# Performance work log

Hardware: AMD Instinct MI355X
Metric: run time of the kernel (lower is better)

Reference implementation:

```python
import jax, jax.numpy as jnp
import numpy as np

IN_DIM = 3
GRID_LEVEL = 7
FEAT_DIMS = 2
HIDDEN = 128
BOUND = 1.0
W0_SINE = 56.0  # n_levels**feature_dims - n_levels = 8**2 - 8
N = 131072


def setup_inputs() -> dict:
    key = jax.random.key(0)
    ks = jax.random.split(key, 10)
    return {
        "in_pos": jax.random.uniform(ks[0], (N, IN_DIM), jnp.float32, -1.0, 1.0),
        "grid_feats": jax.random.uniform(ks[1], (N, IN_DIM + GRID_LEVEL * FEAT_DIMS), jnp.float32),
        "ffn_A": jax.random.normal(ks[2], (GRID_LEVEL, FEAT_DIMS, HIDDEN), jnp.float32) * 5.0,
        "ffn_sigma": jnp.ones((GRID_LEVEL,), jnp.float32),
        "W0": jax.random.uniform(ks[3], (HIDDEN, IN_DIM), jnp.float32, -1.0 / IN_DIM, 1.0 / IN_DIM),
        "b0": jax.random.uniform(ks[4], (HIDDEN,), jnp.float32, -1.0 / IN_DIM, 1.0 / IN_DIM),
        "W_mid": jax.random.uniform(ks[5], (GRID_LEVEL, HIDDEN, HIDDEN), jnp.float32) * (2.0 * np.sqrt(6.0 / HIDDEN) / W0_SINE) - np.sqrt(6.0 / HIDDEN) / W0_SINE,
        "b_mid": jnp.zeros((GRID_LEVEL, HIDDEN), jnp.float32),
        "W_high": jax.random.uniform(ks[6], (GRID_LEVEL, HIDDEN, HIDDEN), jnp.float32) * (2.0 * np.sqrt(6.0 / HIDDEN) / W0_SINE) - np.sqrt(6.0 / HIDDEN) / W0_SINE,
        "b_high": jnp.zeros((GRID_LEVEL, HIDDEN), jnp.float32),
    }


def reference(in_pos, grid_feats, ffn_A, ffn_sigma, W0, b0, W_mid, b_mid, W_high, b_high):
    x = in_pos / BOUND                     # [N, 3], in [-1, 1]
    pos01 = (in_pos + BOUND) / (2.0 * BOUND)  # [N, 3], in [0, 1]

    # grid branch: slice off the first in_dim columns, reshape to [L, N, F]
    gx = grid_feats[..., IN_DIM:].reshape(-1, GRID_LEVEL, FEAT_DIMS).transpose(1, 0, 2)
    A = ffn_A * ffn_sigma[:, None, None]   # [L, F, H]
    grid_x = jnp.sin(jnp.einsum('lnf,lfh->lnh', gx, (2.0 * jnp.pi) * A))  # [L, N, H]

    # first SIREN layer
    x = jnp.sin(W0_SINE * (x @ W0.T + b0))  # [N, H]

    def step(carry, layer):
        x, buf = carry
        Wm, bm, Wh, bh, g = layer
        x = jnp.sin(W0_SINE * (x @ Wm.T + bm))
        x = g + x                                  # residual add of grid features
        buf = buf + jnp.sin(W0_SINE * (x @ Wh.T + bh))  # high-freq accumulation
        return (x, buf), None

    buf0 = jnp.zeros((x.shape[0], HIDDEN), x.dtype)
    (_, buf), _ = jax.lax.scan(step, (x, buf0), (W_mid, b_mid, W_high, b_high, grid_x))

    return jnp.concatenate([pos01, buf / GRID_LEVEL], axis=-1)  # [N, 3 + 128]
```

## Files before the change

### kernel.cpp

```cpp
#include <hip/hip_runtime.h>
#include <hip/hip_bf16.h>


typedef __bf16 bf16_t;
typedef __attribute__((ext_vector_type(8))) __bf16 bf16x8;
typedef __attribute__((ext_vector_type(4))) float f32x4;
typedef __attribute__((ext_vector_type(16))) float f32x16;

#define C56R 8.9126768f
#define INV7 0.14285714285714285f

#define OFF_WMF   0
#define OFF_WMFLO 229376
#define OFF_WHF   458752
#define OFF_EPM   688128

union ChunkU { bf16x8 v; unsigned int d[4]; };

__device__ __forceinline__ unsigned short bfbits(float x) {
  bf16_t b = (bf16_t)x;
  return __builtin_bit_cast(unsigned short, b);
}
__device__ __forceinline__ float bf2f(unsigned short u) {
  return __builtin_bit_cast(float, (unsigned int)u << 16);
}
__device__ __forceinline__ void pack2(float v0, float v1,
                                      unsigned int& ph, unsigned int& pl) {
  unsigned short h0 = bfbits(v0), h1 = bfbits(v1);
  ph = (unsigned int)h0 | ((unsigned int)h1 << 16);
  float l0 = v0 - bf2f(h0), l1 = v1 - bf2f(h1);
  pl = (unsigned int)bfbits(l0) | ((unsigned int)bfbits(l1) << 16);
}

__global__ void ffb_prep(const float* __restrict__ ffnA, const float* __restrict__ sigma,
                         const float* __restrict__ Wm, const float* __restrict__ bm,
                         const float* __restrict__ Wh, const float* __restrict__ bh,
                         unsigned char* __restrict__ ws) {
  int i = blockIdx.x * 256 + threadIdx.x;
  bf16_t* wmf = (bf16_t*)(ws + OFF_WMF);
  bf16_t* wml = (bf16_t*)(ws + OFF_WMFLO);
  bf16_t* whf = (bf16_t*)(ws + OFF_WHF);
  {
    int j    = i & 7;
    int lane = (i >> 3) & 63;
    int kc   = (i >> 9) & 7;
    int mt   = (i >> 12) & 3;
    int it   = i >> 14;
    int ho   = (mt << 5) + (lane & 31);
    int hin  = (kc << 4) + ((lane >> 5) << 3) + j;
    int src  = (it << 14) + (ho << 7) + hin;
    float w  = Wm[src];
    bf16_t h = (bf16_t)w;
    wmf[i] = h;
    wml[i] = (bf16_t)(w - (float)h);
    whf[i] = (bf16_t)Wh[src];
  }
  if (i < 896) {
    int r  = i & 15;
    int mt = (i >> 4) & 3;
    int hf = (i >> 6) & 1;
    int it = i >> 7;
    int h  = (mt << 5) + (r & 3) + ((r >> 2) << 3) + (hf << 2);
    float sg = sigma[it];
    f32x4 e;
    e.x = ffnA[it * 256 + h] * sg;
    e.y = ffnA[it * 256 + 128 + h] * sg;
    e.z = C56R * bm[it * 128 + h];
    e.w = C56R * bh[it * 128 + h];
    ((f32x4*)(ws + OFF_EPM))[i] = e;
  }
}

__launch_bounds__(256, 3)
__global__ void ffb_main(const float* __restrict__ pos,
                         const float* __restrict__ gfeat,
                         const float* __restrict__ W0,
                         const float* __restrict__ b0,
                         const unsigned char* __restrict__ ws,
                         float* __restrict__ out) {
  __shared__ __align__(16) unsigned char smem[48000];
  unsigned char* sX0 = smem;
  f32x4* sEPv = (f32x4*)(smem + 32768);
  float* sEPf = (float*)(smem + 32768);

  const int tid  = threadIdx.x;
  const int L    = tid & 63;
  const int sub  = tid >> 6;
  const int p    = L & 31;
  const int hf   = L >> 5;
  const int n    = (blockIdx.x << 5) + p;

  const bf16_t* __restrict__ WMH = (const bf16_t*)(ws + OFF_WMF);
  const bf16_t* __restrict__ WML = (const bf16_t*)(ws + OFF_WMFLO);
  const bf16_t* __restrict__ WHF = (const bf16_t*)(ws + OFF_WHF);
  const f32x4*  __restrict__ EPM = (const f32x4*)(ws + OFF_EPM);

  bf16x8 mh[8], ml[8], hfr[8];
  {
    const bf16_t* wh0 = WMH + (sub << 12) + (L << 3);
    const bf16_t* wl0 = WML + (sub << 12) + (L << 3);
    #pragma unroll
    for (int kc = 0; kc < 8; ++kc) {
      mh[kc] = *(const bf16x8*)(wh0 + (kc << 9));
      ml[kc] = *(const bf16x8*)(wl0 + (kc << 9));
    }
  }

  #pragma unroll
  for (int c = 0; c < 4; ++c) {
    int idx = tid + (c << 8);
    if (idx < 896) sEPv[(idx >> 4) * 17 + (idx & 15)] = EPM[idx];
  }

  const float p0 = pos[n * 3 + 0], p1 = pos[n * 3 + 1], p2 = pos[n * 3 + 2];
  if (sub == 0 && hf == 0) {
    out[(size_t)n * 131 + 0] = (p0 + 1.f) * 0.5f;
    out[(size_t)n * 131 + 1] = (p1 + 1.f) * 0.5f;
    out[(size_t)n * 131 + 2] = (p2 + 1.f) * 0.5f;
  }

  #pragma unroll
  for (int cc = 0; cc < 2; ++cc) {
    const int c = (sub << 1) + cc;
    ChunkU chi, clo;
    #pragma unroll
    for (int jp = 0; jp < 4; ++jp) {
      int h0 = (c << 4) + (hf << 3) + 2 * jp;
      float d0 = __builtin_fmaf(p2, W0[h0*3+2], __builtin_fmaf(p1, W0[h0*3+1], p0 * W0[h0*3+0]));
      float d1 = __builtin_fmaf(p2, W0[h0*3+5], __builtin_fmaf(p1, W0[h0*3+4], p0 * W0[h0*3+3]));
      float v0 = __builtin_amdgcn_sinf(C56R * (d0 + b0[h0]));
      float v1 = __builtin_amdgcn_sinf(C56R * (d1 + b0[h0 + 1]));
      pack2(v0, v1, chi.d[jp], clo.d[jp]);
    }
    *(bf16x8*)(sX0 + (c << 10) + (L << 4))        = chi.v;
    *(bf16x8*)(sX0 + 8192 + (c << 10) + (L << 4)) = clo.v;
  }
  __syncthreads();

  f32x16 buf;
  #pragma unroll
  for (int r = 0; r < 16; ++r) buf[r] = 0.f;

  #pragma unroll 1
  for (int it = 0; it < 8; ++it) {
    unsigned char* rb = sX0 + ((it & 1) << 14);
    unsigned char* wb = sX0 + (((it + 1) & 1) << 14);

    if (it > 0) {
      f32x16 acc;
      #pragma unroll
      for (int r = 0; r < 16; ++r) acc[r] = 0.f;
      #pragma unroll
      for (int kc = 0; kc < 8; ++kc) {
        bf16x8 xhc = *(const bf16x8*)(rb + (kc << 10) + (L << 4));
        acc = __builtin_amdgcn_mfma_f32_32x32x16_bf16(hfr[kc], xhc, acc, 0, 0, 0);
      }
      const int eb17 = ((((it - 1) << 1) + hf) * 4 + sub) * 17;
      #pragma unroll
      for (int r = 0; r < 16; ++r) {
        float cbh = sEPf[(eb17 + r) * 4 + 3];
        buf[r] += __builtin_amdgcn_sinf(__builtin_fmaf(acc[r], C56R, cbh));
      }
    }

    if (it < 7) {
      {
        const bf16_t* wbp = WHF + (it << 14) + (sub << 12) + (L << 3);
        #pragma unroll
        for (int kc = 0; kc < 8; ++kc)
          hfr[kc] = *(const bf16x8*)(wbp + (kc << 9));
      }

      f32x16 acc;
      #pragma unroll
      for (int r = 0; r < 16; ++r) acc[r] = 0.f;
      #pragma unroll
      for (int kc = 0; kc < 8; ++kc) {
        bf16x8 xhc = *(const bf16x8*)(rb + (kc << 10) + (L << 4));
        bf16x8 xlc = *(const bf16x8*)(rb + 8192 + (kc << 10) + (L << 4));
        acc = __builtin_amdgcn_mfma_f32_32x32x16_bf16(mh[kc], xhc, acc, 0, 0, 0);
        acc = __builtin_amdgcn_mfma_f32_32x32x16_bf16(ml[kc], xhc, acc, 0, 0, 0);
        acc = __builtin_amdgcn_mfma_f32_32x32x16_bf16(mh[kc], xlc, acc, 0, 0, 0);
      }

      if (it < 6) {
        const bf16_t* wh = WMH + ((it + 1) << 14) + (sub << 12) + (L << 3);
        const bf16_t* wl = WML + ((it + 1) << 14) + (sub << 12) + (L << 3);
        #pragma unroll
        for (int kc = 0; kc < 8; ++kc) {
          mh[kc] = *(const bf16x8*)(wh + (kc << 9));
          ml[kc] = *(const bf16x8*)(wl + (kc << 9));
        }
      }

      const float g0 = gfeat[n * 17 + 3 + 2 * it];
      const float g1 = gfeat[n * 17 + 4 + 2 * it];
      const int eb17 = (((it << 1) + hf) * 4 + sub) * 17;
      #pragma unroll
      for (int q = 0; q < 4; ++q) {
        const int r0 = q << 2;
        float v[4];
        #pragma unroll
        for (int k = 0; k < 4; ++k) {
          const int r = r0 + k;
          f32x4 e = sEPv[eb17 + r];
          float sg = __builtin_amdgcn_sinf(__builtin_amdgcn_fractf(__builtin_fmaf(g1, e.y, g0 * e.x)));
          float sm = __builtin_amdgcn_sinf(__builtin_fmaf(acc[r], C56R, e.z));
          v[k] = sg + sm;
        }
        unsigned int ph0, pl0, ph1, pl1;
        pack2(v[0], v[1], ph0, pl0);
        pack2(v[2], v[3], ph1, pl1);
        unsigned long long qh = (unsigned long long)ph0 | ((unsigned long long)ph1 << 32);
        unsigned long long ql = (unsigned long long)pl0 | ((unsigned long long)pl1 << 32);
        const int c   = (sub << 1) + (r0 >> 3);
        const int bit = (r0 >> 2) & 1;
        const int off = (c << 10) + ((p + (bit << 5)) << 4) + (hf << 3);
        *(unsigned long long*)(wb + off)        = qh;
        *(unsigned long long*)(wb + 8192 + off) = ql;
      }
      __syncthreads();
    }
  }

  float* op = out + (size_t)n * 131 + 3;
  #pragma unroll
  for (int r = 0; r < 16; ++r) {
    const int h = (sub << 5) + (r & 3) + ((r >> 2) << 3) + (hf << 2);
    op[h] = buf[r] * INV7;
  }
}

extern "C" void kernel_launch(void* const* d_in, const int* in_sizes, int n_in,
                              void* d_out, int out_size, void* d_ws, size_t ws_size,
                              hipStream_t stream) {
  (void)in_sizes; (void)n_in; (void)out_size; (void)ws_size;
  const float* pos   = (const float*)d_in[0];
  const float* gfeat = (const float*)d_in[1];
  const float* ffnA  = (const float*)d_in[2];
  const float* sigma = (const float*)d_in[3];
  const float* W0    = (const float*)d_in[4];
  const float* b0    = (const float*)d_in[5];
  const float* Wm    = (const float*)d_in[6];
  const float* bm    = (const float*)d_in[7];
  const float* Wh    = (const float*)d_in[8];
  const float* bh    = (const float*)d_in[9];
  float* out = (float*)d_out;
  unsigned char* ws = (unsigned char*)d_ws;

  hipLaunchKernelGGL(ffb_prep, dim3(448), dim3(256), 0, stream,
                     ffnA, sigma, Wm, bm, Wh, bh, ws);
  hipLaunchKernelGGL(ffb_main, dim3(4096), dim3(256), 0, stream,
                     pos, gfeat, W0, b0, ws, out);
}
```

Measured before the change: 267.7 us.

## Process two 32-point tiles per block to reuse weight fragments

Each block now handles 64 points as two 32-point tiles (A and B) that share the same register-resident weight fragments, so each weight load is amortized over twice the MFMA work. Shared memory grows to 64KB for the doubled activation ping-pong buffers, and the bias/FFN epilogue table now comes straight from global memory instead of a shared-memory copy. The high-frequency sine accumulation is deferred to after the next mid-layer MFMAs to overlap with them. Occupancy drops (launch bounds 3 to 2, grid halved) and register pressure rises with twice the accumulators.

```diff
diff --git a/kernel.cpp b/kernel.cpp
--- a/kernel.cpp
+++ b/kernel.cpp
@@ -71,29 +71,28 @@
   }
 }
 
-__launch_bounds__(256, 3)
+__launch_bounds__(256, 2)
 __global__ void ffb_main(const float* __restrict__ pos,
                          const float* __restrict__ gfeat,
                          const float* __restrict__ W0,
                          const float* __restrict__ b0,
                          const unsigned char* __restrict__ ws,
                          float* __restrict__ out) {
-  __shared__ __align__(16) unsigned char smem[48000];
-  unsigned char* sX0 = smem;
-  f32x4* sEPv = (f32x4*)(smem + 32768);
-  float* sEPf = (float*)(smem + 32768);
+  __shared__ __align__(16) unsigned char sX[65536];
 
   const int tid  = threadIdx.x;
   const int L    = tid & 63;
   const int sub  = tid >> 6;
   const int p    = L & 31;
   const int hf   = L >> 5;
-  const int n    = (blockIdx.x << 5) + p;
+  const int nA   = (blockIdx.x << 6) + p;
+  const int nB   = nA + 32;
 
   const bf16_t* __restrict__ WMH = (const bf16_t*)(ws + OFF_WMF);
   const bf16_t* __restrict__ WML = (const bf16_t*)(ws + OFF_WMFLO);
   const bf16_t* __restrict__ WHF = (const bf16_t*)(ws + OFF_WHF);
   const f32x4*  __restrict__ EPM = (const f32x4*)(ws + OFF_EPM);
+  const float*  __restrict__ EPW = (const float*)(ws + OFF_EPM);
 
   bf16x8 mh[8], ml[8], hfr[8];
   {
@@ -106,60 +105,61 @@
     }
   }
 
+  const float pA0 = pos[nA * 3 + 0], pA1 = pos[nA * 3 + 1], pA2 = pos[nA * 3 + 2];
+  const float pB0 = pos[nB * 3 + 0], pB1 = pos[nB * 3 + 1], pB2 = pos[nB * 3 + 2];
+  if (sub == 0 && hf == 0) {
+    out[(size_t)nA * 131 + 0] = (pA0 + 1.f) * 0.5f;
+    out[(size_t)nA * 131 + 1] = (pA1 + 1.f) * 0.5f;
+    out[(size_t)nA * 131 + 2] = (pA2 + 1.f) * 0.5f;
+    out[(size_t)nB * 131 + 0] = (pB0 + 1.f) * 0.5f;
+    out[(size_t)nB * 131 + 1] = (pB1 + 1.f) * 0.5f;
+    out[(size_t)nB * 131 + 2] = (pB2 + 1.f) * 0.5f;
+  }
+
   #pragma unroll
-  for (int c = 0; c < 4; ++c) {
-    int idx = tid + (c << 8);
-    if (idx < 896) sEPv[(idx >> 4) * 17 + (idx & 15)] = EPM[idx];
-  }
-
-  const float p0 = pos[n * 3 + 0], p1 = pos[n * 3 + 1], p2 = pos[n * 3 + 2];
-  if (sub == 0 && hf == 0) {
-    out[(size_t)n * 131 + 0] = (p0 + 1.f) * 0.5f;
-    out[(size_t)n * 131 + 1] = (p1 + 1.f) * 0.5f;
-    out[(size_t)n * 131 + 2] = (p2 + 1.f) * 0.5f;
-  }
-
+  for (int q = 0; q < 2; ++q) {
+    const float q0 = q ? pB0 : pA0;
+    const float q1 = q ? pB1 : pA1;
+    const float q2 = q ? pB2 : pA2;
+    unsigned char* base = sX + (q << 14);
+    #pragma unroll
+    for (int cc = 0; cc < 2; ++cc) {
+      const int c = (sub << 1) + cc;
+      ChunkU chi, clo;
+      #pragma unroll
+      for (int jp = 0; jp < 4; ++jp) {
+        int h0 = (c << 4) + (hf << 3) + 2 * jp;
+        float d0 = __builtin_fmaf(q2, W0[h0*3+2], __builtin_fmaf(q1, W0[h0*3+1], q0 * W0[h0*3+0]));
+        float d1 = __builtin_fmaf(q2, W0[h0*3+5], __builtin_fmaf(q1, W0[h0*3+4], q0 * W0[h0*3+3]));
+        float v0 = __builtin_amdgcn_sinf(C56R * (d0 + b0[h0]));
+        float v1 = __builtin_amdgcn_sinf(C56R * (d1 + b0[h0 + 1]));
+        pack2(v0, v1, chi.d[jp], clo.d[jp]);
+      }
+      *(bf16x8*)(base + (c << 10) + (L << 4))        = chi.v;
+      *(bf16x8*)(base + 8192 + (c << 10) + (L << 4)) = clo.v;
+    }
+  }
+  __syncthreads();
+
+  f32x16 bufA, bufB;
   #pragma unroll
-  for (int cc = 0; cc < 2; ++cc) {
-    const int c = (sub << 1) + cc;
-    ChunkU chi, clo;
-    #pragma unroll
-    for (int jp = 0; jp < 4; ++jp) {
-      int h0 = (c << 4) + (hf << 3) + 2 * jp;
-      float d0 = __builtin_fmaf(p2, W0[h0*3+2], __builtin_fmaf(p1, W0[h0*3+1], p0 * W0[h0*3+0]));
-      float d1 = __builtin_fmaf(p2, W0[h0*3+5], __builtin_fmaf(p1, W0[h0*3+4], p0 * W0[h0*3+3]));
-      float v0 = __builtin_amdgcn_sinf(C56R * (d0 + b0[h0]));
-      float v1 = __builtin_amdgcn_sinf(C56R * (d1 + b0[h0 + 1]));
-      pack2(v0, v1, chi.d[jp], clo.d[jp]);
-    }
-    *(bf16x8*)(sX0 + (c << 10) + (L << 4))        = chi.v;
-    *(bf16x8*)(sX0 + 8192 + (c << 10) + (L << 4)) = clo.v;
-  }
-  __syncthreads();
-
-  f32x16 buf;
-  #pragma unroll
-  for (int r = 0; r < 16; ++r) buf[r] = 0.f;
+  for (int r = 0; r < 16; ++r) { bufA[r] = 0.f; bufB[r] = 0.f; }
 
   #pragma unroll 1
   for (int it = 0; it < 8; ++it) {
-    unsigned char* rb = sX0 + ((it & 1) << 14);
-    unsigned char* wb = sX0 + (((it + 1) & 1) << 14);
-
+    unsigned char* rb  = sX + ((it & 1) << 15);
+    unsigned char* wbf = sX + (((it + 1) & 1) << 15);
+
+    f32x16 accHA, accHB;
     if (it > 0) {
-      f32x16 acc;
-      #pragma unroll
-      for (int r = 0; r < 16; ++r) acc[r] = 0.f;
+      #pragma unroll
+      for (int r = 0; r < 16; ++r) { accHA[r] = 0.f; accHB[r] = 0.f; }
       #pragma unroll
       for (int kc = 0; kc < 8; ++kc) {
-        bf16x8 xhc = *(const bf16x8*)(rb + (kc << 10) + (L << 4));
-        acc = __builtin_amdgcn_mfma_f32_32x32x16_bf16(hfr[kc], xhc, acc, 0, 0, 0);
-      }
-      const int eb17 = ((((it - 1) << 1) + hf) * 4 + sub) * 17;
-      #pragma unroll
-      for (int r = 0; r < 16; ++r) {
-        float cbh = sEPf[(eb17 + r) * 4 + 3];
-        buf[r] += __builtin_amdgcn_sinf(__builtin_fmaf(acc[r], C56R, cbh));
+        bf16x8 xA = *(const bf16x8*)(rb + (kc << 10) + (L << 4));
+        bf16x8 xB = *(const bf16x8*)(rb + 16384 + (kc << 10) + (L << 4));
+        accHA = __builtin_amdgcn_mfma_f32_32x32x16_bf16(hfr[kc], xA, accHA, 0, 0, 0);
+        accHB = __builtin_amdgcn_mfma_f32_32x32x16_bf16(hfr[kc], xB, accHB, 0, 0, 0);
       }
     }
 
@@ -171,16 +171,24 @@
           hfr[kc] = *(const bf16x8*)(wbp + (kc << 9));
       }
 
-      f32x16 acc;
-      #pragma unroll
-      for (int r = 0; r < 16; ++r) acc[r] = 0.f;
+      f32x16 accA, accB;
+      #pragma unroll
+      for (int r = 0; r < 16; ++r) { accA[r] = 0.f; accB[r] = 0.f; }
       #pragma unroll
       for (int kc = 0; kc < 8; ++kc) {
-        bf16x8 xhc = *(const bf16x8*)(rb + (kc << 10) + (L << 4));
-        bf16x8 xlc = *(const bf16x8*)(rb + 8192 + (kc << 10) + (L << 4));
-        acc = __builtin_amdgcn_mfma_f32_32x32x16_bf16(mh[kc], xhc, acc, 0, 0, 0);
-        acc = __builtin_amdgcn_mfma_f32_32x32x16_bf16(ml[kc], xhc, acc, 0, 0, 0);
-        acc = __builtin_amdgcn_mfma_f32_32x32x16_bf16(mh[kc], xlc, acc, 0, 0, 0);
+        bf16x8 xhA = *(const bf16x8*)(rb + (kc << 10) + (L << 4));
+        bf16x8 xlA = *(const bf16x8*)(rb + 8192 + (kc << 10) + (L << 4));
+        accA = __builtin_amdgcn_mfma_f32_32x32x16_bf16(mh[kc], xhA, accA, 0, 0, 0);
+        accA = __builtin_amdgcn_mfma_f32_32x32x16_bf16(ml[kc], xhA, accA, 0, 0, 0);
+        accA = __builtin_amdgcn_mfma_f32_32x32x16_bf16(mh[kc], xlA, accA, 0, 0, 0);
+      }
+      #pragma unroll
+      for (int kc = 0; kc < 8; ++kc) {
+        bf16x8 xhB = *(const bf16x8*)(rb + 16384 + (kc << 10) + (L << 4));
+        bf16x8 xlB = *(const bf16x8*)(rb + 24576 + (kc << 10) + (L << 4));
+        accB = __builtin_amdgcn_mfma_f32_32x32x16_bf16(mh[kc], xhB, accB, 0, 0, 0);
+        accB = __builtin_amdgcn_mfma_f32_32x32x16_bf16(ml[kc], xhB, accB, 0, 0, 0);
+        accB = __builtin_amdgcn_mfma_f32_32x32x16_bf16(mh[kc], xlB, accB, 0, 0, 0);
       }
 
       if (it < 6) {
@@ -193,41 +201,72 @@
         }
       }
 
-      const float g0 = gfeat[n * 17 + 3 + 2 * it];
-      const float g1 = gfeat[n * 17 + 4 + 2 * it];
-      const int eb17 = (((it << 1) + hf) * 4 + sub) * 17;
+      if (it > 0) {
+        const int ebp = ((((it - 1) << 1) + hf) * 4 + sub) * 16;
+        #pragma unroll
+        for (int r = 0; r < 16; ++r) {
+          float cbh = EPW[(ebp + r) * 4 + 3];
+          bufA[r] += __builtin_amdgcn_sinf(__builtin_fmaf(accHA[r], C56R, cbh));
+          bufB[r] += __builtin_amdgcn_sinf(__builtin_fmaf(accHB[r], C56R, cbh));
+        }
+      }
+
+      const float g0A = gfeat[nA * 17 + 3 + 2 * it];
+      const float g1A = gfeat[nA * 17 + 4 + 2 * it];
+      const float g0B = gfeat[nB * 17 + 3 + 2 * it];
+      const float g1B = gfeat[nB * 17 + 4 + 2 * it];
+      const int eb = (((it << 1) + hf) * 4 + sub) * 16;
       #pragma unroll
       for (int q = 0; q < 4; ++q) {
         const int r0 = q << 2;
-        float v[4];
+        float vA[4], vB[4];
         #pragma unroll
         for (int k = 0; k < 4; ++k) {
           const int r = r0 + k;
-          f32x4 e = sEPv[eb17 + r];
-          float sg = __builtin_amdgcn_sinf(__builtin_amdgcn_fractf(__builtin_fmaf(g1, e.y, g0 * e.x)));
-          float sm = __builtin_amdgcn_sinf(__builtin_fmaf(acc[r], C56R, e.z));
-          v[k] = sg + sm;
+          f32x4 e = EPM[eb + r];
+          float sgA = __builtin_amdgcn_sinf(__builtin_amdgcn_fractf(__builtin_fmaf(g1A, e.y, g0A * e.x)));
+          float smA = __builtin_amdgcn_sinf(__builtin_fmaf(accA[r], C56R, e.z));
+          vA[k] = sgA + smA;
+          float sgB = __builtin_amdgcn_sinf(__builtin_amdgcn_fractf(__builtin_fmaf(g1B, e.y, g0B * e.x)));
+          float smB = __builtin_amdgcn_sinf(__builtin_fmaf(accB[r], C56R, e.z));
+          vB[k] = sgB + smB;
         }
-        unsigned int ph0, pl0, ph1, pl1;
-        pack2(v[0], v[1], ph0, pl0);
-        pack2(v[2], v[3], ph1, pl1);
-        unsigned long long qh = (unsigned long long)ph0 | ((unsigned long long)ph1 << 32);
-        unsigned long long ql = (unsigned long long)pl0 | ((unsigned long long)pl1 << 32);
+        unsigned int h0, l0, h1, l1;
+        pack2(vA[0], vA[1], h0, l0);
+        pack2(vA[2], vA[3], h1, l1);
+        unsigned long long qhA = (unsigned long long)h0 | ((unsigned long long)h1 << 32);
+        unsigned long long qlA = (unsigned long long)l0 | ((unsigned long long)l1 << 32);
+        pack2(vB[0], vB[1], h0, l0);
+        pack2(vB[2], vB[3], h1, l1);
+        unsigned long long qhB = (unsigned long long)h0 | ((unsigned long long)h1 << 32);
+        unsigned long long qlB = (unsigned long long)l0 | ((unsigned long long)l1 << 32);
         const int c   = (sub << 1) + (r0 >> 3);
         const int bit = (r0 >> 2) & 1;
         const int off = (c << 10) + ((p + (bit << 5)) << 4) + (hf << 3);
-        *(unsigned long long*)(wb + off)        = qh;
-        *(unsigned long long*)(wb + 8192 + off) = ql;
+        *(unsigned long long*)(wbf + off)                = qhA;
+        *(unsigned long long*)(wbf + 8192 + off)         = qlA;
+        *(unsigned long long*)(wbf + 16384 + off)        = qhB;
+        *(unsigned long long*)(wbf + 24576 + off)        = qlB;
       }
       __syncthreads();
-    }
-  }
-
-  float* op = out + (size_t)n * 131 + 3;
+    } else {
+      const int ebp = ((((it - 1) << 1) + hf) * 4 + sub) * 16;
+      #pragma unroll
+      for (int r = 0; r < 16; ++r) {
+        float cbh = EPW[(ebp + r) * 4 + 3];
+        bufA[r] += __builtin_amdgcn_sinf(__builtin_fmaf(accHA[r], C56R, cbh));
+        bufB[r] += __builtin_amdgcn_sinf(__builtin_fmaf(accHB[r], C56R, cbh));
+      }
+    }
+  }
+
+  float* opA = out + (size_t)nA * 131 + 3;
+  float* opB = out + (size_t)nB * 131 + 3;
   #pragma unroll
   for (int r = 0; r < 16; ++r) {
     const int h = (sub << 5) + (r & 3) + ((r >> 2) << 3) + (hf << 2);
-    op[h] = buf[r] * INV7;
+    opA[h] = bufA[r] * INV7;
+    opB[h] = bufB[r] * INV7;
   }
 }
 
@@ -250,6 +289,6 @@
 
   hipLaunchKernelGGL(ffb_prep, dim3(448), dim3(256), 0, stream,
                      ffnA, sigma, Wm, bm, Wh, bh, ws);
-  hipLaunchKernelGGL(ffb_main, dim3(4096), dim3(256), 0, stream,
+  hipLaunchKernelGGL(ffb_main, dim3(2048), dim3(256), 0, stream,
                      pos, gfeat, W0, b0, ws, out);
 }
```

Measured after the change: 508.7 us. +90.1%, slower.

## Peel first and last iterations and fuse high and mid MFMA chains

Applied to the files above, without the earlier changes.

The layer loop is restructured: iteration 0 and the final high-frequency step are peeled out, and the middle iterations issue the previous layer's high-frequency MFMA and the current layer's mid MFMA chain in one interleaved loop over shared LDS reads. This lets the X tile be read once for both products and gives the MFMA pipe two independent accumulator chains to overlap. Weight reloads are moved after both chains. It needs an extra live 16-float accumulator, which adds register pressure.

```diff
diff --git a/kernel.cpp b/kernel.cpp
--- a/kernel.cpp
+++ b/kernel.cpp
@@ -141,85 +141,156 @@
   #pragma unroll
   for (int r = 0; r < 16; ++r) buf[r] = 0.f;
 
+  {
+    unsigned char* rb = sX0;
+    unsigned char* wb = sX0 + 16384;
+
+    {
+      const bf16_t* wbp = WHF + (sub << 12) + (L << 3);
+      #pragma unroll
+      for (int kc = 0; kc < 8; ++kc)
+        hfr[kc] = *(const bf16x8*)(wbp + (kc << 9));
+    }
+
+    f32x16 accM;
+    #pragma unroll
+    for (int r = 0; r < 16; ++r) accM[r] = 0.f;
+    #pragma unroll
+    for (int kc = 0; kc < 8; ++kc) {
+      bf16x8 xhc = *(const bf16x8*)(rb + (kc << 10) + (L << 4));
+      bf16x8 xlc = *(const bf16x8*)(rb + 8192 + (kc << 10) + (L << 4));
+      accM = __builtin_amdgcn_mfma_f32_32x32x16_bf16(mh[kc], xhc, accM, 0, 0, 0);
+      accM = __builtin_amdgcn_mfma_f32_32x32x16_bf16(ml[kc], xhc, accM, 0, 0, 0);
+      accM = __builtin_amdgcn_mfma_f32_32x32x16_bf16(mh[kc], xlc, accM, 0, 0, 0);
+    }
+
+    {
+      const bf16_t* wh = WMH + (1 << 14) + (sub << 12) + (L << 3);
+      const bf16_t* wl = WML + (1 << 14) + (sub << 12) + (L << 3);
+      #pragma unroll
+      for (int kc = 0; kc < 8; ++kc) {
+        mh[kc] = *(const bf16x8*)(wh + (kc << 9));
+        ml[kc] = *(const bf16x8*)(wl + (kc << 9));
+      }
+    }
+
+    const float g0 = gfeat[n * 17 + 3];
+    const float g1 = gfeat[n * 17 + 4];
+    const int eb17 = ((hf) * 4 + sub) * 17;
+    #pragma unroll
+    for (int q = 0; q < 4; ++q) {
+      const int r0 = q << 2;
+      float v[4];
+      #pragma unroll
+      for (int k = 0; k < 4; ++k) {
+        const int r = r0 + k;
+        f32x4 e = sEPv[eb17 + r];
+        float sg = __builtin_amdgcn_sinf(__builtin_amdgcn_fractf(__builtin_fmaf(g1, e.y, g0 * e.x)));
+        float sm = __builtin_amdgcn_sinf(__builtin_fmaf(accM[r], C56R, e.z));
+        v[k] = sg + sm;
+      }
+      unsigned int ph0, pl0, ph1, pl1;
+      pack2(v[0], v[1], ph0, pl0);
+      pack2(v[2], v[3], ph1, pl1);
+      unsigned long long qh = (unsigned long long)ph0 | ((unsigned long long)ph1 << 32);
+      unsigned long long ql = (unsigned long long)pl0 | ((unsigned long long)pl1 << 32);
+      const int c   = (sub << 1) + (r0 >> 3);
+      const int bit = (r0 >> 2) & 1;
+      const int off = (c << 10) + ((p + (bit << 5)) << 4) + (hf << 3);
+      *(unsigned long long*)(wb + off)        = qh;
+      *(unsigned long long*)(wb + 8192 + off) = ql;
+    }
+    __syncthreads();
+  }
+
   #pragma unroll 1
-  for (int it = 0; it < 8; ++it) {
+  for (int it = 1; it < 7; ++it) {
     unsigned char* rb = sX0 + ((it & 1) << 14);
     unsigned char* wb = sX0 + (((it + 1) & 1) << 14);
 
-    if (it > 0) {
-      f32x16 acc;
-      #pragma unroll
-      for (int r = 0; r < 16; ++r) acc[r] = 0.f;
+    f32x16 accH, accM;
+    #pragma unroll
+    for (int r = 0; r < 16; ++r) { accH[r] = 0.f; accM[r] = 0.f; }
+
+    #pragma unroll
+    for (int kc = 0; kc < 8; ++kc) {
+      bf16x8 xhc = *(const bf16x8*)(rb + (kc << 10) + (L << 4));
+      bf16x8 xlc = *(const bf16x8*)(rb + 8192 + (kc << 10) + (L << 4));
+      accH = __builtin_amdgcn_mfma_f32_32x32x16_bf16(hfr[kc], xhc, accH, 0, 0, 0);
+      accM = __builtin_amdgcn_mfma_f32_32x32x16_bf16(mh[kc],  xhc, accM, 0, 0, 0);
+      accM = __builtin_amdgcn_mfma_f32_32x32x16_bf16(ml[kc],  xhc, accM, 0, 0, 0);
+      accM = __builtin_amdgcn_mfma_f32_32x32x16_bf16(mh[kc],  xlc, accM, 0, 0, 0);
+    }
+
+    {
+      const bf16_t* wbp = WHF + (it << 14) + (sub << 12) + (L << 3);
+      #pragma unroll
+      for (int kc = 0; kc < 8; ++kc)
+        hfr[kc] = *(const bf16x8*)(wbp + (kc << 9));
+    }
+    if (it < 6) {
+      const bf16_t* wh = WMH + ((it + 1) << 14) + (sub << 12) + (L << 3);
+      const bf16_t* wl = WML + ((it + 1) << 14) + (sub << 12) + (L << 3);
       #pragma unroll
       for (int kc = 0; kc < 8; ++kc) {
-        bf16x8 xhc = *(const bf16x8*)(rb + (kc << 10) + (L << 4));
-        acc = __builtin_amdgcn_mfma_f32_32x32x16_bf16(hfr[kc], xhc, acc, 0, 0, 0);
-      }
-      const int eb17 = ((((it - 1) << 1) + hf) * 4 + sub) * 17;
+        mh[kc] = *(const bf16x8*)(wh + (kc << 9));
+        ml[kc] = *(const bf16x8*)(wl + (kc << 9));
+      }
+    }
+
+    {
+      const int ebp17 = ((((it - 1) << 1) + hf) * 4 + sub) * 17;
       #pragma unroll
       for (int r = 0; r < 16; ++r) {
-        float cbh = sEPf[(eb17 + r) * 4 + 3];
-        buf[r] += __builtin_amdgcn_sinf(__builtin_fmaf(acc[r], C56R, cbh));
-      }
-    }
-
-    if (it < 7) {
-      {
-        const bf16_t* wbp = WHF + (it << 14) + (sub << 12) + (L << 3);
-        #pragma unroll
-        for (int kc = 0; kc < 8; ++kc)
-          hfr[kc] = *(const bf16x8*)(wbp + (kc << 9));
-      }
-
-      f32x16 acc;
-      #pragma unroll
-      for (int r = 0; r < 16; ++r) acc[r] = 0.f;
-      #pragma unroll
-      for (int kc = 0; kc < 8; ++kc) {
-        bf16x8 xhc = *(const bf16x8*)(rb + (kc << 10) + (L << 4));
-        bf16x8 xlc = *(const bf16x8*)(rb + 8192 + (kc << 10) + (L << 4));
-        acc = __builtin_amdgcn_mfma_f32_32x32x16_bf16(mh[kc], xhc, acc, 0, 0, 0);
-        acc = __builtin_amdgcn_mfma_f32_32x32x16_bf16(ml[kc], xhc, acc, 0, 0, 0);
-        acc = __builtin_amdgcn_mfma_f32_32x32x16_bf16(mh[kc], xlc, acc, 0, 0, 0);
-      }
-
-      if (it < 6) {
-        const bf16_t* wh = WMH + ((it + 1) << 14) + (sub << 12) + (L << 3);
-        const bf16_t* wl = WML + ((it + 1) << 14) + (sub << 12) + (L << 3);
-        #pragma unroll
-        for (int kc = 0; kc < 8; ++kc) {
-          mh[kc] = *(const bf16x8*)(wh + (kc << 9));
-          ml[kc] = *(const bf16x8*)(wl + (kc << 9));
-        }
-      }
-
-      const float g0 = gfeat[n * 17 + 3 + 2 * it];
-      const float g1 = gfeat[n * 17 + 4 + 2 * it];
-      const int eb17 = (((it << 1) + hf) * 4 + sub) * 17;
-      #pragma unroll
-      for (int q = 0; q < 4; ++q) {
-        const int r0 = q << 2;
-        float v[4];
-        #pragma unroll
-        for (int k = 0; k < 4; ++k) {
-          const int r = r0 + k;
-          f32x4 e = sEPv[eb17 + r];
-          float sg = __builtin_amdgcn_sinf(__builtin_amdgcn_fractf(__builtin_fmaf(g1, e.y, g0 * e.x)));
-          float sm = __builtin_amdgcn_sinf(__builtin_fmaf(acc[r], C56R, e.z));
-          v[k] = sg + sm;
-        }
-        unsigned int ph0, pl0, ph1, pl1;
-        pack2(v[0], v[1], ph0, pl0);
-        pack2(v[2], v[3], ph1, pl1);
-        unsigned long long qh = (unsigned long long)ph0 | ((unsigned long long)ph1 << 32);
-        unsigned long long ql = (unsigned long long)pl0 | ((unsigned long long)pl1 << 32);
-        const int c   = (sub << 1) + (r0 >> 3);
-        const int bit = (r0 >> 2) & 1;
-        const int off = (c << 10) + ((p + (bit << 5)) << 4) + (hf << 3);
-        *(unsigned long long*)(wb + off)        = qh;
-        *(unsigned long long*)(wb + 8192 + off) = ql;
-      }
-      __syncthreads();
+        float cbh = sEPf[(ebp17 + r) * 4 + 3];
+        buf[r] += __builtin_amdgcn_sinf(__builtin_fmaf(accH[r], C56R, cbh));
+      }
+    }
+
+    const float g0 = gfeat[n * 17 + 3 + 2 * it];
+    const float g1 = gfeat[n * 17 + 4 + 2 * it];
+    const int eb17 = (((it << 1) + hf) * 4 + sub) * 17;
+    #pragma unroll
+    for (int q = 0; q < 4; ++q) {
+      const int r0 = q << 2;
+      float v[4];
+      #pragma unroll
+      for (int k = 0; k < 4; ++k) {
+        const int r = r0 + k;
+        f32x4 e = sEPv[eb17 + r];
+        float sg = __builtin_amdgcn_sinf(__builtin_amdgcn_fractf(__builtin_fmaf(g1, e.y, g0 * e.x)));
+        float sm = __builtin_amdgcn_sinf(__builtin_fmaf(accM[r], C56R, e.z));
+        v[k] = sg + sm;
+      }
+      unsigned int ph0, pl0, ph1, pl1;
+      pack2(v[0], v[1], ph0, pl0);
+      pack2(v[2], v[3], ph1, pl1);
+      unsigned long long qh = (unsigned long long)ph0 | ((unsigned long long)ph1 << 32);
+      unsigned long long ql = (unsigned long long)pl0 | ((unsigned long long)pl1 << 32);
+      const int c   = (sub << 1) + (r0 >> 3);
+      const int bit = (r0 >> 2) & 1;
+      const int off = (c << 10) + ((p + (bit << 5)) << 4) + (hf << 3);
+      *(unsigned long long*)(wb + off)        = qh;
+      *(unsigned long long*)(wb + 8192 + off) = ql;
+    }
+    __syncthreads();
+  }
+
+  {
+    unsigned char* rb = sX0 + 16384;
+    f32x16 accH;
+    #pragma unroll
+    for (int r = 0; r < 16; ++r) accH[r] = 0.f;
+    #pragma unroll
+    for (int kc = 0; kc < 8; ++kc) {
+      bf16x8 xhc = *(const bf16x8*)(rb + (kc << 10) + (L << 4));
+      accH = __builtin_amdgcn_mfma_f32_32x32x16_bf16(hfr[kc], xhc, accH, 0, 0, 0);
+    }
+    const int ebp17 = (((6 << 1) + hf) * 4 + sub) * 17;
+    #pragma unroll
+    for (int r = 0; r < 16; ++r) {
+      float cbh = sEPf[(ebp17 + r) * 4 + 3];
+      buf[r] += __builtin_amdgcn_sinf(__builtin_fmaf(accH[r], C56R, cbh));
     }
   }
 
```

Result: slower. 300.1 us (+12.1%).
